# Kernel optimization log

Measured on AMD Instinct MI355X. Metric: run time of the kernel, lower is better.

## Reference

```python
import jax, jax.numpy as jnp
import numpy as np

NQ = 6          # num_qubits
BS = 3          # basis_size (Pauli x,y,z)
HID = 32        # LSTM hidden size
SNAPS = 16      # max_num_snapshots
BATCH = 1024
DIM = 2 ** NQ   # 64


def _pauli():
    sx = np.array([[0., 1.], [1., 0.]], dtype=np.complex64)
    sy = np.array([[0., -1j], [1j, 0.]], dtype=np.complex64)
    sz = np.array([[1., 0.], [0., -1.]], dtype=np.complex64)
    return np.stack([sx, sy, sz], axis=0)


def setup_inputs():
    key = jax.random.key(0)
    ks = jax.random.split(key, 12)
    snapshot = jax.random.uniform(ks[0], (BATCH, NQ), jnp.float32, -1.0, 1.0)
    basis_comp_vector = jax.nn.softmax(
        jax.random.normal(ks[1], (BATCH, NQ, BS), jnp.float32), axis=-1)
    # valid density matrices: rho = A A^dag / tr
    ar = jax.random.normal(ks[2], (BATCH, DIM, DIM), jnp.float32)
    ai = jax.random.normal(ks[3], (BATCH, DIM, DIM), jnp.float32)
    A = ar + 1j * ai
    rho_c = jnp.einsum('bij,bkj->bik', A, jnp.conj(A))
    tr = jnp.trace(rho_c, axis1=1, axis2=2)[:, None, None]
    rho_c = rho_c / tr
    rho = jnp.stack([jnp.real(rho_c), jnp.imag(rho_c)], axis=1).astype(jnp.float32)
    h0 = jax.random.normal(ks[4], (BATCH, HID), jnp.float32)
    c0 = jax.random.normal(ks[5], (BATCH, HID), jnp.float32)
    in_dim = NQ + NQ * BS
    W_ih = jax.random.normal(ks[6], (4 * HID, in_dim), jnp.float32) * 0.1
    W_hh = jax.random.normal(ks[7], (4 * HID, HID), jnp.float32) * 0.1
    b_ih = jax.random.normal(ks[8], (4 * HID,), jnp.float32) * 0.05
    b_hh = jax.random.normal(ks[9], (4 * HID,), jnp.float32) * 0.05
    Wp = jax.random.normal(ks[10], (NQ, HID, BS), jnp.float32) * 0.1
    bp = jax.random.normal(ks[11], (NQ, BS), jnp.float32) * 0.05
    pauli = _pauli()
    basis_r = jnp.asarray(np.real(pauli), jnp.float32)
    basis_i = jnp.asarray(np.imag(pauli), jnp.float32)
    return {"snapshot": snapshot, "basis_comp_vector": basis_comp_vector,
            "rho": rho, "h0": h0, "c0": c0,
            "W_ih": W_ih, "W_hh": W_hh, "b_ih": b_ih, "b_hh": b_hh,
            "Wp": Wp, "bp": bp, "basis_r": basis_r, "basis_i": basis_i}


def _apply(p, M, axis, b):
    # apply 2x2 batched operator M [b,2,2] on tensor axis `axis` of p [b]+(2,)*2NQ
    pm = jnp.moveaxis(p, axis, 1)
    shp = pm.shape
    out = jnp.einsum('bij,bjr->bir', M, pm.reshape(b, 2, -1)).reshape(shp)
    return jnp.moveaxis(out, 1, axis)


def _measure(rho_t, probs, basis, basis_c, b):
    # sequential single-qubit measurement on the collapsing mixed state
    pc = probs.astype(jnp.complex64)
    M = jnp.einsum('bqs,sij->bqij', pc, basis)    # prob-mixed basis ops
    Mc = jnp.einsum('bqs,sij->bqij', pc, basis_c)
    p = rho_t
    outs = []
    for q in range(NQ):
        p = _apply(p, M[:, q], 1 + q, b)          # row index of qubit q
        p = _apply(p, Mc[:, q], 1 + NQ + q, b)    # col index of qubit q
        tr = jnp.trace(p.reshape(b, DIM, DIM), axis1=1, axis2=2)
        outs.append(jnp.real(tr))                 # measurement value s
        p = p / tr.reshape((b,) + (1,) * (2 * NQ))  # renormalized post-state
    return jnp.stack(outs, axis=1)                 # [b, NQ]


def _forward(snapshot, basis_comp_vector, rho, h0, c0,
             W_ih, W_hh, b_ih, b_hh, Wp, bp, basis_r, basis_i):
    b = snapshot.shape[0]
    basis = (basis_r + 1j * basis_i).astype(jnp.complex64)
    basis_c = jnp.conj(basis)
    rho_t = (rho[:, 0] + 1j * rho[:, 1]).astype(jnp.complex64)
    rho_t = rho_t.reshape((b,) + (2,) * (2 * NQ))

    x = jnp.concatenate([snapshot, basis_comp_vector.reshape(b, -1)], axis=-1)
    feats = [x]
    h, c = h0, c0
    for _ in range(SNAPS - 1):
        # torch LSTMCell: gate order i, f, g, o
        g = x @ W_ih.T + b_ih + h @ W_hh.T + b_hh
        gi, gf, gg, go = jnp.split(g, 4, axis=-1)
        c = jax.nn.sigmoid(gf) * c + jax.nn.sigmoid(gi) * jnp.tanh(gg)
        h = jax.nn.sigmoid(go) * jnp.tanh(c)
        probs = jax.nn.softmax(jnp.einsum('bh,qhs->bqs', h, Wp) + bp, axis=-1)
        # torch.Tensor(snapshot_batch) detaches -> stop_gradient
        snaps = jax.lax.stop_gradient(_measure(rho_t, probs, basis, basis_c, b))
        x = jnp.concatenate([snaps, probs.reshape(b, -1)], axis=-1)
        feats.append(x)

    # classical-shadow reconstruction: kron_q (I + 3 s_q B_q)/2, averaged
    eye2 = jnp.eye(2, dtype=jnp.complex64)
    acc = jnp.zeros((b, DIM, DIM), jnp.complex64)
    last_bv = None
    for xw in feats:
        shadow = xw[:, :NQ]
        bv = xw[:, NQ:].reshape(b, NQ, BS)
        last_bv = bv
        Bq = jnp.einsum('bqs,sij->bqij', bv.astype(jnp.complex64), basis)
        rc = (eye2 + 3.0 * shadow[:, :, None, None].astype(jnp.complex64) * Bq) / 2.0
        k = rc[:, 0]
        dd = 2
        for q in range(1, NQ):  # batched kron chain
            k = jnp.einsum('bij,bkl->bikjl', k, rc[:, q]).reshape(b, dd * 2, dd * 2)
            dd *= 2
        acc = acc + k
    rho_rec = acc / SNAPS
    out = jnp.stack([jnp.real(rho_rec), jnp.imag(rho_rec)], axis=1)
    return out, last_bv


def reference(snapshot, basis_comp_vector, rho, h0, c0,
              W_ih, W_hh, b_ih, b_hh, Wp, bp, basis_r, basis_i):
    return _forward(snapshot, basis_comp_vector, rho, h0, c0,
                    W_ih, W_hh, b_ih, b_hh, Wp, bp, basis_r, basis_i)
```

## Files before the change

kernel.cpp:

```cpp
#include <hip/hip_runtime.h>

#define NQ 6
#define HID 32
#define SNAPS 16
#define BATCH 1024
#define FSTRIDE 24
#define FTOT 384
#define KSTR 24
#define KF   192
#define WSTR 416

typedef float vfloat4 __attribute__((ext_vector_type(4)));

__device__ __forceinline__ float sigm_f(float x) { return 1.0f / (1.0f + __expf(-x)); }
__device__ __forceinline__ float tanh_f(float x) { return 1.0f - 2.0f / (__expf(2.0f * x) + 1.0f); }

__device__ __forceinline__ void rc_entry(float g, float b0, float b1, float b2,
                                         int i, int j, float& re, float& im) {
    if (i == j) { re = 0.5f + (i ? -g * b2 : g * b2); im = 0.0f; }
    else        { re = g * b0;  im = (i ? g * b1 : -g * b1); }
}

__global__ __launch_bounds__(256, 1)
void lstm_kernel(const float* __restrict__ snapshot,
                 const float* __restrict__ bcv,
                 const float* __restrict__ h0,
                 const float* __restrict__ c0,
                 const float* __restrict__ W_ih,
                 const float* __restrict__ W_hh,
                 const float* __restrict__ b_ih,
                 const float* __restrict__ b_hh,
                 const float* __restrict__ Wp,
                 const float* __restrict__ bp,
                 float* __restrict__ feats,
                 float* __restrict__ out_tail)
{
    __shared__ __align__(16) float sbuf[4 * WSTR];
    const int w = threadIdx.x >> 6;
    const int l = threadIdx.x & 63;
    const int b = blockIdx.x * 4 + w;
    float* feat = sbuf + w * WSTR;
    float* sh   = feat + 384;

    float4 wih0[6], wih1[6], whh0[8], whh1[8];
    {
        const float4* p0 = (const float4*)(W_ih + l * 24);
        const float4* p1 = (const float4*)(W_ih + (l + 64) * 24);
        #pragma unroll
        for (int k = 0; k < 6; ++k) { wih0[k] = p0[k]; wih1[k] = p1[k]; }
        const float4* q0 = (const float4*)(W_hh + l * 32);
        const float4* q1 = (const float4*)(W_hh + (l + 64) * 32);
        #pragma unroll
        for (int k = 0; k < 8; ++k) { whh0[k] = q0[k]; whh1[k] = q1[k]; }
    }
    const float bias0 = b_ih[l] + b_hh[l];
    const float bias1 = b_ih[l + 64] + b_hh[l + 64];

    float wp[32];
    float bpv = 0.0f;
    if (l < 18) {
        int q = l / 3, s = l - 3 * q;
        #pragma unroll
        for (int k = 0; k < 32; ++k) wp[k] = Wp[q * 96 + 3 * k + s];
        bpv = bp[l];
    }

    float c = 0.0f;
    if (l < 32) { c = c0[b * 32 + l]; sh[l] = h0[b * 32 + l]; }
    if (l < 24) feat[l] = (l < 6) ? snapshot[b * 6 + l] : bcv[b * 18 + (l - 6)];
    __builtin_amdgcn_wave_barrier();

    for (int step = 0; step < SNAPS - 1; ++step) {
        const float4* x4 = (const float4*)(feat + step * FSTRIDE);
        const float4* h4 = (const float4*)sh;
        float g0 = bias0, g1 = bias1, g0b = 0.0f, g1b = 0.0f;
        #pragma unroll
        for (int k = 0; k < 6; ++k) {
            float4 xq = x4[k];
            g0  += xq.x * wih0[k].x + xq.y * wih0[k].y;
            g0b += xq.z * wih0[k].z + xq.w * wih0[k].w;
            g1  += xq.x * wih1[k].x + xq.y * wih1[k].y;
            g1b += xq.z * wih1[k].z + xq.w * wih1[k].w;
        }
        #pragma unroll
        for (int k = 0; k < 8; ++k) {
            float4 hq = h4[k];
            g0  += hq.x * whh0[k].x + hq.y * whh0[k].y;
            g0b += hq.z * whh0[k].z + hq.w * whh0[k].w;
            g1  += hq.x * whh1[k].x + hq.y * whh1[k].y;
            g1b += hq.z * whh1[k].z + hq.w * whh1[k].w;
        }
        g0 += g0b; g1 += g1b;

        float gf = __shfl_xor(g0, 32);
        float go = __shfl_xor(g1, 32);
        if (l < 32) {
            c = sigm_f(gf) * c + sigm_f(g0) * tanh_f(g1);
            sh[l] = sigm_f(go) * tanh_f(c);
        }
        __builtin_amdgcn_wave_barrier();

        float logit = bpv;
        const float4* h4b = (const float4*)sh;
        #pragma unroll
        for (int k = 0; k < 8; ++k) {
            float4 hq = h4b[k];
            logit += hq.x * wp[4 * k] + hq.y * wp[4 * k + 1]
                   + hq.z * wp[4 * k + 2] + hq.w * wp[4 * k + 3];
        }

        int q3 = 3 * (l < 6 ? l : 0);
        float l0 = __shfl(logit, q3), l1 = __shfl(logit, q3 + 1), l2 = __shfl(logit, q3 + 2);
        if (l < 6) {
            float m = fmaxf(l0, fmaxf(l1, l2));
            float e0 = __expf(l0 - m), e1 = __expf(l1 - m), e2 = __expf(l2 - m);
            float inv = 1.0f / (e0 + e1 + e2);
            float p0 = e0 * inv, p1 = e1 * inv, p2 = e2 * inv;
            float snap = p0 * p0 + p1 * p1 + p2 * p2;
            float* fd = feat + (step + 1) * FSTRIDE;
            fd[l] = snap;
            fd[6 + 3 * l]     = p0;
            fd[6 + 3 * l + 1] = p1;
            fd[6 + 3 * l + 2] = p2;
        }
        __builtin_amdgcn_wave_barrier();
    }

    #pragma unroll
    for (int k = 0; k < 6; ++k)
        feats[b * FTOT + k * 64 + l] = feat[k * 64 + l];
    if (l < 18) out_tail[b * 18 + l] = feat[15 * FSTRIDE + 6 + l];
}

__global__ __launch_bounds__(256, 2)
void recon_kernel(const float* __restrict__ feats, float* __restrict__ out)
{
    __shared__ __align__(16) float sK[2 * 16 * KF + FTOT];
    float* sKA = sK;
    float* sKB = sK + 16 * KF;
    float* sf  = sK + 32 * KF;
    const int b = blockIdx.x;
    const int t = threadIdx.x;

    sf[t] = feats[b * FTOT + t];
    if (t < 128) sf[256 + t] = feats[b * FTOT + 256 + t];
    __syncthreads();

    for (int n = t; n < 2048; n += 256) {
        int f = n >> 7, r = n & 127;
        int half = r >> 6, a = r & 63;
        const float* fx = &sf[f * FSTRIDE];
        int i0 = (a >> 5) & 1, i1 = (a >> 4) & 1, i2 = (a >> 3) & 1;
        int j0 = (a >> 2) & 1, j1 = (a >> 1) & 1, j2 = a & 1;
        int q = 3 * half;
        float g0 = 1.5f * fx[q], g1 = 1.5f * fx[q + 1], g2 = 1.5f * fx[q + 2];
        const float* bb = fx + 6 + 3 * q;
        float r0, m0, r1, m1, r2, m2;
        rc_entry(g0, bb[0], bb[1], bb[2], i0, j0, r0, m0);
        rc_entry(g1, bb[3], bb[4], bb[5], i1, j1, r1, m1);
        rc_entry(g2, bb[6], bb[7], bb[8], i2, j2, r2, m2);
        float pr = r0 * r1 - m0 * m1, pi = r0 * m1 + m0 * r1;
        float qr = pr * r2 - pi * m2, qi = pr * m2 + pi * r2;
        int row = a >> 3, col = a & 7;
        if (half == 0) {
            int off = f * KF + col * KSTR + ((row & 1) ? (7 + row) : row);
            sKA[off] = qr; sKA[off + 1] = qi;
        } else {
            int off = f * KF + row * KSTR + 2 * col;
            sKB[off] = qr; sKB[off + 1] = qi;
        }
    }
    __syncthreads();

    const int u = t & 15, v = t >> 4;
    const float* baseA = sKA + (u >> 1) * KSTR + 8 * (v >> 3);
    const float* baseB = sKB + (v & 7) * KSTR + 8 * (u & 1);
    float accr[4][4], acci[4][4];
    #pragma unroll
    for (int e = 0; e < 4; ++e)
        #pragma unroll
        for (int d = 0; d < 4; ++d) { accr[e][d] = 0.0f; acci[e][d] = 0.0f; }

    #pragma unroll 2
    for (int f = 0; f < SNAPS; ++f) {
        float4 A0 = *(const float4*)(baseA + f * KF);
        float4 A1 = *(const float4*)(baseA + f * KF + 4);
        float4 B0 = *(const float4*)(baseB + f * KF);
        float4 B1 = *(const float4*)(baseB + f * KF + 4);
        float ar[4] = {A0.x, A0.z, A1.x, A1.z};
        float ai[4] = {A0.y, A0.w, A1.y, A1.w};
        float br[4] = {B0.x, B0.z, B1.x, B1.z};
        float bi[4] = {B0.y, B0.w, B1.y, B1.w};
        #pragma unroll
        for (int e = 0; e < 4; ++e)
            #pragma unroll
            for (int d = 0; d < 4; ++d) {
                accr[e][d] += ar[e] * br[d] - ai[e] * bi[d];
                acci[e][d] += ar[e] * bi[d] + ai[e] * br[d];
            }
    }

    const float s = 1.0f / 16.0f;
    float* outb = out + (size_t)b * 8192;
    #pragma unroll
    for (int e = 0; e < 4; ++e) {
        int i = v + 16 * e;
        vfloat4 r4 = { accr[e][0] * s, accr[e][1] * s, accr[e][2] * s, accr[e][3] * s };
        vfloat4 i4 = { acci[e][0] * s, acci[e][1] * s, acci[e][2] * s, acci[e][3] * s };
        __builtin_nontemporal_store(r4, (vfloat4*)(outb + i * 64 + 4 * u));
        __builtin_nontemporal_store(i4, (vfloat4*)(outb + 4096 + i * 64 + 4 * u));
    }
}

extern "C" void kernel_launch(void* const* d_in, const int* in_sizes, int n_in,
                              void* d_out, int out_size, void* d_ws, size_t ws_size,
                              hipStream_t stream) {
    const float* snapshot = (const float*)d_in[0];
    const float* bcv      = (const float*)d_in[1];
    const float* h0       = (const float*)d_in[3];
    const float* c0       = (const float*)d_in[4];
    const float* W_ih     = (const float*)d_in[5];
    const float* W_hh     = (const float*)d_in[6];
    const float* b_ih     = (const float*)d_in[7];
    const float* b_hh     = (const float*)d_in[8];
    const float* Wp       = (const float*)d_in[9];
    const float* bp       = (const float*)d_in[10];
    float* out   = (float*)d_out;
    float* featw = (float*)d_ws;

    lstm_kernel<<<BATCH / 4, 256, 0, stream>>>(
        snapshot, bcv, h0, c0, W_ih, W_hh, b_ih, b_hh, Wp, bp,
        featw, out + (size_t)BATCH * 8192);
    recon_kernel<<<BATCH, 256, 0, stream>>>(featw, out);
}
```

Baseline: 134.4 us.

## Fuse LSTM recurrence and shadow reconstruction into one per-sample kernel

Merges the LSTM kernel and the reconstruction kernel into one kernel with one block per batch element. The features stay in shared memory instead of going through a global workspace, which removes a launch and the feature round trip. The LSTM step now spreads the 128 gate rows over 128 threads and uses block-wide __syncthreads between phases, where the old code had one wave per sample with shuffles. The recurrence is serial and leaves most of the 256 threads idle, and it now runs inside every recon block, so block latency grows.

```diff
diff --git a/kernel.cpp b/kernel.cpp
--- a/kernel.cpp
+++ b/kernel.cpp
@@ -8,7 +8,6 @@
 #define FTOT 384
 #define KSTR 24
 #define KF   192
-#define WSTR 416
 
 typedef float vfloat4 __attribute__((ext_vector_type(4)));
 
@@ -21,135 +20,112 @@
     else        { re = g * b0;  im = (i ? g * b1 : -g * b1); }
 }
 
-__global__ __launch_bounds__(256, 1)
-void lstm_kernel(const float* __restrict__ snapshot,
-                 const float* __restrict__ bcv,
-                 const float* __restrict__ h0,
-                 const float* __restrict__ c0,
-                 const float* __restrict__ W_ih,
-                 const float* __restrict__ W_hh,
-                 const float* __restrict__ b_ih,
-                 const float* __restrict__ b_hh,
-                 const float* __restrict__ Wp,
-                 const float* __restrict__ bp,
-                 float* __restrict__ feats,
-                 float* __restrict__ out_tail)
+__global__ __launch_bounds__(256, 2)
+void fused_kernel(const float* __restrict__ snapshot,
+                  const float* __restrict__ bcv,
+                  const float* __restrict__ h0,
+                  const float* __restrict__ c0,
+                  const float* __restrict__ W_ih,
+                  const float* __restrict__ W_hh,
+                  const float* __restrict__ b_ih,
+                  const float* __restrict__ b_hh,
+                  const float* __restrict__ Wp,
+                  const float* __restrict__ bp,
+                  float* __restrict__ out,
+                  float* __restrict__ out_tail)
 {
-    __shared__ __align__(16) float sbuf[4 * WSTR];
-    const int w = threadIdx.x >> 6;
-    const int l = threadIdx.x & 63;
-    const int b = blockIdx.x * 4 + w;
-    float* feat = sbuf + w * WSTR;
-    float* sh   = feat + 384;
-
-    float4 wih0[6], wih1[6], whh0[8], whh1[8];
-    {
-        const float4* p0 = (const float4*)(W_ih + l * 24);
-        const float4* p1 = (const float4*)(W_ih + (l + 64) * 24);
-        #pragma unroll
-        for (int k = 0; k < 6; ++k) { wih0[k] = p0[k]; wih1[k] = p1[k]; }
-        const float4* q0 = (const float4*)(W_hh + l * 32);
-        const float4* q1 = (const float4*)(W_hh + (l + 64) * 32);
-        #pragma unroll
-        for (int k = 0; k < 8; ++k) { whh0[k] = q0[k]; whh1[k] = q1[k]; }
-    }
-    const float bias0 = b_ih[l] + b_hh[l];
-    const float bias1 = b_ih[l + 64] + b_hh[l + 64];
-
-    float wp[32];
-    float bpv = 0.0f;
-    if (l < 18) {
-        int q = l / 3, s = l - 3 * q;
-        #pragma unroll
-        for (int k = 0; k < 32; ++k) wp[k] = Wp[q * 96 + 3 * k + s];
-        bpv = bp[l];
-    }
-
-    float c = 0.0f;
-    if (l < 32) { c = c0[b * 32 + l]; sh[l] = h0[b * 32 + l]; }
-    if (l < 24) feat[l] = (l < 6) ? snapshot[b * 6 + l] : bcv[b * 18 + (l - 6)];
-    __builtin_amdgcn_wave_barrier();
-
-    for (int step = 0; step < SNAPS - 1; ++step) {
-        const float4* x4 = (const float4*)(feat + step * FSTRIDE);
-        const float4* h4 = (const float4*)sh;
-        float g0 = bias0, g1 = bias1, g0b = 0.0f, g1b = 0.0f;
-        #pragma unroll
-        for (int k = 0; k < 6; ++k) {
-            float4 xq = x4[k];
-            g0  += xq.x * wih0[k].x + xq.y * wih0[k].y;
-            g0b += xq.z * wih0[k].z + xq.w * wih0[k].w;
-            g1  += xq.x * wih1[k].x + xq.y * wih1[k].y;
-            g1b += xq.z * wih1[k].z + xq.w * wih1[k].w;
-        }
-        #pragma unroll
-        for (int k = 0; k < 8; ++k) {
-            float4 hq = h4[k];
-            g0  += hq.x * whh0[k].x + hq.y * whh0[k].y;
-            g0b += hq.z * whh0[k].z + hq.w * whh0[k].w;
-            g1  += hq.x * whh1[k].x + hq.y * whh1[k].y;
-            g1b += hq.z * whh1[k].z + hq.w * whh1[k].w;
-        }
-        g0 += g0b; g1 += g1b;
-
-        float gf = __shfl_xor(g0, 32);
-        float go = __shfl_xor(g1, 32);
-        if (l < 32) {
-            c = sigm_f(gf) * c + sigm_f(g0) * tanh_f(g1);
-            sh[l] = sigm_f(go) * tanh_f(c);
-        }
-        __builtin_amdgcn_wave_barrier();
-
-        float logit = bpv;
-        const float4* h4b = (const float4*)sh;
-        #pragma unroll
-        for (int k = 0; k < 8; ++k) {
-            float4 hq = h4b[k];
-            logit += hq.x * wp[4 * k] + hq.y * wp[4 * k + 1]
-                   + hq.z * wp[4 * k + 2] + hq.w * wp[4 * k + 3];
-        }
-
-        int q3 = 3 * (l < 6 ? l : 0);
-        float l0 = __shfl(logit, q3), l1 = __shfl(logit, q3 + 1), l2 = __shfl(logit, q3 + 2);
-        if (l < 6) {
-            float m = fmaxf(l0, fmaxf(l1, l2));
-            float e0 = __expf(l0 - m), e1 = __expf(l1 - m), e2 = __expf(l2 - m);
-            float inv = 1.0f / (e0 + e1 + e2);
-            float p0 = e0 * inv, p1 = e1 * inv, p2 = e2 * inv;
-            float snap = p0 * p0 + p1 * p1 + p2 * p2;
-            float* fd = feat + (step + 1) * FSTRIDE;
-            fd[l] = snap;
-            fd[6 + 3 * l]     = p0;
-            fd[6 + 3 * l + 1] = p1;
-            fd[6 + 3 * l + 2] = p2;
-        }
-        __builtin_amdgcn_wave_barrier();
-    }
-
-    #pragma unroll
-    for (int k = 0; k < 6; ++k)
-        feats[b * FTOT + k * 64 + l] = feat[k * 64 + l];
-    if (l < 18) out_tail[b * 18 + l] = feat[15 * FSTRIDE + 6 + l];
-}
-
-__global__ __launch_bounds__(256, 2)
-void recon_kernel(const float* __restrict__ feats, float* __restrict__ out)
-{
-    __shared__ __align__(16) float sK[2 * 16 * KF + FTOT];
-    float* sKA = sK;
-    float* sKB = sK + 16 * KF;
-    float* sf  = sK + 32 * KF;
+    __shared__ __align__(16) float sKA[16 * KF];
+    __shared__ __align__(16) float sKB[16 * KF];
+    __shared__ __align__(16) float feat[FTOT];
+    __shared__ __align__(16) float sh[HID];
+    __shared__ __align__(16) float sg[128];
+
     const int b = blockIdx.x;
     const int t = threadIdx.x;
 
-    sf[t] = feats[b * FTOT + t];
-    if (t < 128) sf[256 + t] = feats[b * FTOT + 256 + t];
+    float4 wih[6], whh[8];
+    float bias = 0.0f;
+    if (t < 128) {
+        const float4* p = (const float4*)(W_ih + t * 24);
+        #pragma unroll
+        for (int k = 0; k < 6; ++k) wih[k] = p[k];
+        const float4* q = (const float4*)(W_hh + t * 32);
+        #pragma unroll
+        for (int k = 0; k < 8; ++k) whh[k] = q[k];
+        bias = b_ih[t] + b_hh[t];
+    }
+    float wp[32];
+    float bpv = 0.0f, c = 0.0f;
+    if (t < 18) {
+        int q = t / 3, s = t - 3 * q;
+        #pragma unroll
+        for (int k = 0; k < 32; ++k) wp[k] = Wp[q * 96 + 3 * k + s];
+        bpv = bp[t];
+    }
+    if (t < 32) { c = c0[b * 32 + t]; sh[t] = h0[b * 32 + t]; }
+    if (t < 24) feat[t] = (t < 6) ? snapshot[b * 6 + t] : bcv[b * 18 + (t - 6)];
     __syncthreads();
+
+    for (int step = 0; step < SNAPS - 1; ++step) {
+        if (t < 128) {
+            const float4* x4 = (const float4*)(feat + step * FSTRIDE);
+            const float4* h4 = (const float4*)sh;
+            float ga = bias, gb = 0.0f;
+            #pragma unroll
+            for (int k = 0; k < 6; ++k) {
+                float4 xq = x4[k];
+                ga += xq.x * wih[k].x + xq.y * wih[k].y;
+                gb += xq.z * wih[k].z + xq.w * wih[k].w;
+            }
+            #pragma unroll
+            for (int k = 0; k < 8; ++k) {
+                float4 hq = h4[k];
+                ga += hq.x * whh[k].x + hq.y * whh[k].y;
+                gb += hq.z * whh[k].z + hq.w * whh[k].w;
+            }
+            sg[t] = ga + gb;
+        }
+        __syncthreads();
+
+        if (t < 64) {
+            if (t < 32) {
+                float gi = sg[t], gf = sg[32 + t], gg = sg[64 + t], go = sg[96 + t];
+                c = sigm_f(gf) * c + sigm_f(gi) * tanh_f(gg);
+                sh[t] = sigm_f(go) * tanh_f(c);
+            }
+            __builtin_amdgcn_wave_barrier();
+            float logit = bpv;
+            const float4* h4b = (const float4*)sh;
+            #pragma unroll
+            for (int k = 0; k < 8; ++k) {
+                float4 hq = h4b[k];
+                logit += hq.x * wp[4 * k] + hq.y * wp[4 * k + 1]
+                       + hq.z * wp[4 * k + 2] + hq.w * wp[4 * k + 3];
+            }
+            int q3 = 3 * (t < 6 ? t : 0);
+            float l0 = __shfl(logit, q3), l1 = __shfl(logit, q3 + 1), l2 = __shfl(logit, q3 + 2);
+            if (t < 6) {
+                float m = fmaxf(l0, fmaxf(l1, l2));
+                float e0 = __expf(l0 - m), e1 = __expf(l1 - m), e2 = __expf(l2 - m);
+                float inv = 1.0f / (e0 + e1 + e2);
+                float p0 = e0 * inv, p1 = e1 * inv, p2 = e2 * inv;
+                float snap = p0 * p0 + p1 * p1 + p2 * p2;
+                float* fd = feat + (step + 1) * FSTRIDE;
+                fd[t] = snap;
+                fd[6 + 3 * t]     = p0;
+                fd[6 + 3 * t + 1] = p1;
+                fd[6 + 3 * t + 2] = p2;
+            }
+        }
+        __syncthreads();
+    }
+
+    if (t < 18) out_tail[b * 18 + t] = feat[15 * FSTRIDE + 6 + t];
 
     for (int n = t; n < 2048; n += 256) {
         int f = n >> 7, r = n & 127;
         int half = r >> 6, a = r & 63;
-        const float* fx = &sf[f * FSTRIDE];
+        const float* fx = &feat[f * FSTRIDE];
         int i0 = (a >> 5) & 1, i1 = (a >> 4) & 1, i2 = (a >> 3) & 1;
         int j0 = (a >> 2) & 1, j1 = (a >> 1) & 1, j2 = a & 1;
         int q = 3 * half;
@@ -225,11 +201,9 @@
     const float* b_hh     = (const float*)d_in[8];
     const float* Wp       = (const float*)d_in[9];
     const float* bp       = (const float*)d_in[10];
-    float* out   = (float*)d_out;
-    float* featw = (float*)d_ws;
-
-    lstm_kernel<<<BATCH / 4, 256, 0, stream>>>(
+    float* out = (float*)d_out;
+
+    fused_kernel<<<BATCH, 256, 0, stream>>>(
         snapshot, bcv, h0, c0, W_ih, W_hh, b_ih, b_hh, Wp, bp,
-        featw, out + (size_t)BATCH * 8192);
-    recon_kernel<<<BATCH, 256, 0, stream>>>(featw, out);
+        out, out + (size_t)BATCH * 8192);
 }
```

Result: faster. 131.2 us (-2.4%).
